# Optimization experiments

Measured on AMD Instinct MI355X. Metric: run time of the kernel, lower is better.

The kernel has to match this reference:

```python
import jax, jax.numpy as jnp
import numpy as np

N_HEAD = 16
SCALE = True


def setup_inputs() -> dict:
    key = jax.random.key(0)
    k1, k2, k3 = jax.random.split(key, 3)
    B, S, D = 4, 2048, 1024
    x = jax.random.normal(k1, (B, S, D), dtype=jnp.float32)
    w_attn = jax.random.normal(k2, (D, 3 * D), dtype=jnp.float32) * 0.02
    b_attn = jnp.zeros((3 * D,), dtype=jnp.float32)
    w_proj = jax.random.normal(k3, (D, D), dtype=jnp.float32) * 0.02
    b_proj = jnp.zeros((D,), dtype=jnp.float32)
    return {"x": x, "w_attn": w_attn, "b_attn": b_attn, "w_proj": w_proj, "b_proj": b_proj}


def reference(x, w_attn, b_attn, w_proj, b_proj):
    B, S, D = x.shape
    H = N_HEAD
    hd = D // H
    qkv = x @ w_attn + b_attn  # [B,S,3D] (Conv1D)
    q, k, v = jnp.split(qkv, 3, axis=-1)
    # split heads -> [B,H,S,hd]
    q = q.reshape(B, S, H, hd).transpose(0, 2, 1, 3)
    k = k.reshape(B, S, H, hd).transpose(0, 2, 1, 3)
    v = v.reshape(B, S, H, hd).transpose(0, 2, 1, 3)
    w = jnp.einsum('bhqd,bhkd->bhqk', q, k)  # [B,H,S,S]
    if SCALE:
        w = w / jnp.sqrt(jnp.asarray(hd, dtype=w.dtype))
    # causal mask exactly as in source: w*b + -10000*(1-b)
    bmask = jnp.tril(jnp.ones((S, S), dtype=w.dtype))[None, None]
    w = w * bmask + (-10000.0) * (1.0 - bmask)
    w = jax.nn.softmax(w, axis=-1)
    a = jnp.einsum('bhqk,bhkd->bhqd', w, v)  # [B,H,S,hd]
    a = a.transpose(0, 2, 1, 3).reshape(B, S, D)  # merge heads
    out = a @ w_proj + b_proj
    return out
```

## Files before the change

kernel.cpp:

```cpp
#include <hip/hip_runtime.h>

typedef __attribute__((ext_vector_type(8))) _Float16 f16x8;
typedef __attribute__((ext_vector_type(2))) __fp16 h16x2;
typedef __attribute__((ext_vector_type(4))) float f32x4;

#define S_LEN 2048
#define DMODEL 1024
#define NHEAD 16
#define HD 64
#define QKV_LD 3072
#define BTOT 4
#define LOG2E 1.4426950408889634f

#define GLL16(g, l)                                              \
  __builtin_amdgcn_global_load_lds(                              \
      (const __attribute__((address_space(1))) void*)(g),        \
      (__attribute__((address_space(3))) void*)(l), 16, 0, 0)

#define MFMA16(a, b, c) __builtin_amdgcn_mfma_f32_16x16x32_f16(a, b, c, 0, 0, 0)

__global__ __launch_bounds__(256) void cvt_f32_f16_k(const float* __restrict__ in,
                                                     _Float16* __restrict__ out, int n) {
  int i = (blockIdx.x * 256 + threadIdx.x) * 4;
  int stride = gridDim.x * 256 * 4;
  for (; i < n; i += stride) {
    float4 v = *(const float4*)(in + i);
    _Float16 h[4];
    h[0] = (_Float16)v.x; h[1] = (_Float16)v.y; h[2] = (_Float16)v.z; h[3] = (_Float16)v.w;
    *(uint2*)(out + i) = *(const uint2*)h;
  }
}

__global__ __launch_bounds__(256) void transpose_cvt_k(const float* __restrict__ W,
                                                       _Float16* __restrict__ Wt,
                                                       int K, int N) {
  __shared__ float t[32][33];
  int n0 = blockIdx.x * 32, k0 = blockIdx.y * 32;
  int tx = threadIdx.x, ty = threadIdx.y;
#pragma unroll
  for (int i = 0; i < 32; i += 8)
    t[ty + i][tx] = W[(size_t)(k0 + ty + i) * N + n0 + tx];
  __syncthreads();
#pragma unroll
  for (int i = 0; i < 32; i += 8)
    Wt[(size_t)(n0 + ty + i) * K + k0 + tx] = (_Float16)t[tx][ty + i];
}

template <int OUT_F32>
__global__ __launch_bounds__(256) void gemm_bt_k(const _Float16* __restrict__ A,
                                                 const _Float16* __restrict__ Bt,
                                                 const float* __restrict__ bias,
                                                 void* __restrict__ C,
                                                 int M, int N, int K) {
  __shared__ _Float16 As[128 * 64];
  __shared__ _Float16 Bs[128 * 64];
  const int tid = threadIdx.x;
  const int wid = tid >> 6, lane = tid & 63;
  const int quad = lane >> 4, l16 = lane & 15;
  const int wr = wid >> 1, wc = wid & 1;

  const int lin = blockIdx.y * gridDim.x + blockIdx.x;
  const int width = 8 * gridDim.x;
  const int group = lin / width;
  const int pm = group * 8 + (lin % width) % 8;
  const int pn = (lin % width) / 8;
  const int tm = pm * 128, tn = pn * 128;

  const int row0 = tid >> 3;
  const int xc = 8 * ((tid & 7) ^ (row0 & 7));
  const _Float16* Ag = A + (size_t)(tm + row0) * K + xc;
  const _Float16* Bg = Bt + (size_t)(tn + row0) * K + xc;
  _Float16* AsW = &As[wid * 512];
  _Float16* BsW = &Bs[wid * 512];

  f32x4 acc[4][4] = {};

  for (int k0 = 0; k0 < K; k0 += 64) {
    __syncthreads();
#pragma unroll
    for (int p = 0; p < 4; p++) {
      GLL16(Ag + k0 + (size_t)(32 * p) * K, AsW + 2048 * p);
      GLL16(Bg + k0 + (size_t)(32 * p) * K, BsW + 2048 * p);
    }
    __syncthreads();

#pragma unroll
    for (int ks = 0; ks < 2; ks++) {
      f16x8 af[4], bf[4];
#pragma unroll
      for (int mt = 0; mt < 4; mt++)
        af[mt] = *(const f16x8*)&As[(wr * 64 + mt * 16 + l16) * 64 +
                                    (((ks * 4 + quad) ^ (l16 & 7)) << 3)];
#pragma unroll
      for (int nt = 0; nt < 4; nt++)
        bf[nt] = *(const f16x8*)&Bs[(wc * 64 + nt * 16 + l16) * 64 +
                                    (((ks * 4 + quad) ^ (l16 & 7)) << 3)];
#pragma unroll
      for (int mt = 0; mt < 4; mt++)
#pragma unroll
        for (int nt = 0; nt < 4; nt++)
          acc[mt][nt] = MFMA16(af[mt], bf[nt], acc[mt][nt]);
    }
  }

#pragma unroll
  for (int nt = 0; nt < 4; nt++) {
    int col = tn + wc * 64 + nt * 16 + l16;
    float bv = bias[col];
#pragma unroll
    for (int mt = 0; mt < 4; mt++) {
      int row = tm + wr * 64 + mt * 16 + quad * 4;
#pragma unroll
      for (int r = 0; r < 4; r++) {
        float v = acc[mt][nt][r] + bv;
        if (OUT_F32)
          ((float*)C)[(size_t)(row + r) * N + col] = v;
        else
          ((_Float16*)C)[(size_t)(row + r) * N + col] = (_Float16)v;
      }
    }
  }
}

__global__ __launch_bounds__(512, 4) void attn_k(const _Float16* __restrict__ qkv,
                                                 _Float16* __restrict__ out) {
  __shared__ __align__(16) char pool[53760];
  _Float16* KsB = (_Float16*)pool;
  _Float16* VTsB = (_Float16*)(pool + 16384);

  const int tid = threadIdx.x, wid = tid >> 6, lane = tid & 63;
  const int quad = lane >> 4, l16 = lane & 15;
  const int qg = wid & 3, kg = wid >> 2;
  _Float16* PsW = (_Float16*)(pool + 32768) + wid * 1280;
  const int bh = blockIdx.x, b = bh >> 4, h = bh & 15;
  const int p = blockIdx.y;
  const _Float16* base = qkv + (size_t)b * S_LEN * QKV_LD + h * HD;

  const int krow = tid >> 3;
  const _Float16* Kg = base + DMODEL + (size_t)krow * QKV_LD +
                       8 * ((tid & 7) ^ (krow & 7));
  const bool vstager = (tid < 256);
  const int kp = tid & 31, dbase = ((tid >> 5) & 7) * 8;
  const _Float16* Vg = base + 2 * DMODEL + (size_t)(2 * kp) * QKV_LD + dbase;

  int voff[8];
#pragma unroll
  for (int i = 0; i < 8; i++) {
    int d = dbase + i;
    voff[i] = d * 32 + (((kp >> 2) ^ (d & 7)) << 2) + (kp & 3);
  }

  auto stage_V = [&](int bufi, uint4 v0, uint4 v1) {
    union { uint4 u; _Float16 h[8]; } a, c;
    a.u = v0; c.u = v1;
    uint* VT32 = (uint*)(VTsB + bufi * 4096);
#pragma unroll
    for (int i = 0; i < 8; i++) {
      union { _Float16 h[2]; uint u; } w;
      w.h[0] = a.h[i]; w.h[1] = c.h[i];
      VT32[voff[i]] = w.u;
    }
  };

  auto run_pass = [&](int qt) {
    f16x8 bq[2][2];
    {
      const _Float16 qs = (_Float16)(0.125f * LOG2E);
#pragma unroll
      for (int nt = 0; nt < 2; nt++)
#pragma unroll
        for (int ks = 0; ks < 2; ks++) {
          union { uint4 u; f16x8 h; } v;
          v.u = *(const uint4*)(base +
                                (size_t)(qt + qg * 32 + nt * 16 + l16) * QKV_LD +
                                ks * 32 + quad * 8);
          bq[nt][ks] = v.h * qs;
        }
    }

    float l_i[2] = {0.f, 0.f};
    f32x4 o[4][2] = {};

    const int qmin_w = qt + qg * 32;
    const int qmax_w = qmin_w + 31;
    const int nj = qt / 64 + 2;

    __syncthreads();
    GLL16(Kg, KsB + wid * 512);
    if (vstager) stage_V(0, *(const uint4*)(Vg), *(const uint4*)(Vg + QKV_LD));
    __syncthreads();

    for (int j = 0; j < nj; j++) {
      const int cur = j & 1, nxt = cur ^ 1;
      const int k0g = j * 64;
      const bool pf = (j + 1 < nj);
      uint4 pv0, pv1;
      if (pf) {
        const int kn = k0g + 64;
        GLL16(Kg + (size_t)kn * QKV_LD, KsB + nxt * 4096 + wid * 512);
        if (vstager) {
          pv0 = *(const uint4*)(Vg + (size_t)kn * QKV_LD);
          pv1 = *(const uint4*)(Vg + (size_t)(kn + 1) * QKV_LD);
        }
      }

      const int kgbase = k0g + kg * 32;
      if (kgbase <= qmax_w) {
        const _Float16* Kc = KsB + cur * 4096;
        f32x4 sc[2][2];
#pragma unroll
        for (int mt = 0; mt < 2; mt++)
#pragma unroll
          for (int nt = 0; nt < 2; nt++)
            sc[mt][nt] = f32x4{-4.f, -4.f, -4.f, -4.f};
#pragma unroll
        for (int ks = 0; ks < 2; ks++)
#pragma unroll
          for (int mt = 0; mt < 2; mt++) {
            f16x8 ak = *(const f16x8*)&Kc[(kg * 32 + mt * 16 + l16) * 64 +
                                          (((ks * 4 + quad) ^ (l16 & 7)) << 3)];
            sc[mt][0] = MFMA16(ak, bq[0][ks], sc[mt][0]);
            sc[mt][1] = MFMA16(ak, bq[1][ks], sc[mt][1]);
          }

        const bool need_mask = (kgbase + 31 > qmin_w);
#pragma unroll
        for (int nt = 0; nt < 2; nt++) {
          const int qgl = qmin_w + nt * 16 + l16;
          float pe[8];
#pragma unroll
          for (int mt = 0; mt < 2; mt++)
#pragma unroll
            for (int r = 0; r < 4; r++) {
              float v = sc[mt][nt][r];
              if (need_mask) {
                int kgi = kgbase + mt * 16 + quad * 4 + r;
                v = (kgi <= qgl) ? v : -3.0e38f;
              }
              pe[mt * 4 + r] = __builtin_amdgcn_exp2f(v);
            }
          l_i[nt] += ((pe[0] + pe[1]) + (pe[2] + pe[3])) +
                     ((pe[4] + pe[5]) + (pe[6] + pe[7]));
#pragma unroll
          for (int mt = 0; mt < 2; mt++) {
            union { h16x2 h[2]; uint2 u; } w;
            w.h[0] = __builtin_amdgcn_cvt_pkrtz(pe[mt * 4 + 0], pe[mt * 4 + 1]);
            w.h[1] = __builtin_amdgcn_cvt_pkrtz(pe[mt * 4 + 2], pe[mt * 4 + 3]);
            *(uint2*)&PsW[(nt * 16 + l16) * 40 + mt * 16 + quad * 4] = w.u;
          }
        }

        const _Float16* Vc = VTsB + cur * 4096;
        f16x8 bp0 = *(const f16x8*)&PsW[l16 * 40 + quad * 8];
        f16x8 bp1 = *(const f16x8*)&PsW[(16 + l16) * 40 + quad * 8];
#pragma unroll
        for (int md = 0; md < 4; md++) {
          f16x8 av = *(const f16x8*)&Vc[(md * 16 + l16) * 64 +
                                        (((kg * 4 + quad) ^ (l16 & 7)) << 3)];
          o[md][0] = MFMA16(av, bp0, o[md][0]);
          o[md][1] = MFMA16(av, bp1, o[md][1]);
        }
      }

      if (pf && vstager) stage_V(nxt, pv0, pv1);
      __syncthreads();
    }

#pragma unroll
    for (int nt = 0; nt < 2; nt++) {
      float r = l_i[nt];
      r += __shfl_xor(r, 16, 64);
      r += __shfl_xor(r, 32, 64);
      l_i[nt] = r;
    }
    float* X = (float*)pool;
    float* ML = (float*)(pool + 53248);
    if (kg == 1) {
#pragma unroll
      for (int md = 0; md < 4; md++)
#pragma unroll
        for (int nt = 0; nt < 2; nt++)
          *(f32x4*)&X[qg * 2048 + (md * 2 + nt) * 256 + lane * 4] = o[md][nt];
      if (quad == 0) {
#pragma unroll
        for (int nt = 0; nt < 2; nt++)
          ML[(qg * 2 + nt) * 16 + l16] = l_i[nt];
      }
    }
    __syncthreads();
    if (kg == 0) {
      _Float16* PsE = (_Float16*)(pool + 32768) + qg * 2304;
      float inv[2];
#pragma unroll
      for (int nt = 0; nt < 2; nt++)
        inv[nt] = 1.0f / (l_i[nt] + ML[(qg * 2 + nt) * 16 + l16]);
#pragma unroll
      for (int md = 0; md < 4; md++)
#pragma unroll
        for (int nt = 0; nt < 2; nt++) {
          f32x4 o1 = *(const f32x4*)&X[qg * 2048 + (md * 2 + nt) * 256 + lane * 4];
          f32x4 ot = o[md][nt] + o1;
          union { h16x2 h[2]; uint2 u; } w;
          w.h[0] = __builtin_amdgcn_cvt_pkrtz(ot[0] * inv[nt], ot[1] * inv[nt]);
          w.h[1] = __builtin_amdgcn_cvt_pkrtz(ot[2] * inv[nt], ot[3] * inv[nt]);
          *(uint2*)&PsE[(nt * 16 + l16) * 72 + md * 16 + quad * 4] = w.u;
        }
      {
        int r = lane >> 1, ch = (lane & 1) * 32;
        const int qgl = qt + qg * 32 + r;
        _Float16* orow = out + (size_t)(b * S_LEN + qgl) * DMODEL + h * HD + ch;
#pragma unroll
        for (int i = 0; i < 4; i++)
          *(uint4*)(orow + i * 8) = *(const uint4*)&PsE[r * 72 + ch + i * 8];
      }
    }
  };

  run_pass(p * 128);
  run_pass((15 - p) * 128);
}

extern "C" void kernel_launch(void* const* d_in, const int* in_sizes, int n_in,
                              void* d_out, int out_size, void* d_ws, size_t ws_size,
                              hipStream_t stream) {
  const float* x = (const float*)d_in[0];
  const float* w_attn = (const float*)d_in[1];
  const float* b_attn = (const float*)d_in[2];
  const float* w_proj = (const float*)d_in[3];
  const float* b_proj = (const float*)d_in[4];
  float* outp = (float*)d_out;

  char* ws = (char*)d_ws;
  _Float16* x16 = (_Float16*)ws;
  _Float16* wTa = (_Float16*)(ws + 16777216);
  _Float16* wTp = (_Float16*)(ws + 16777216 + 6291456);
  _Float16* qkv = (_Float16*)(ws + 25165824);
  _Float16* abuf = (_Float16*)(ws + 75497472);

  const int nx = BTOT * S_LEN * DMODEL;

  cvt_f32_f16_k<<<8192, 256, 0, stream>>>(x, x16, nx);
  transpose_cvt_k<<<dim3(QKV_LD / 32, DMODEL / 32), dim3(32, 8), 0, stream>>>(
      w_attn, wTa, DMODEL, QKV_LD);
  transpose_cvt_k<<<dim3(DMODEL / 32, DMODEL / 32), dim3(32, 8), 0, stream>>>(
      w_proj, wTp, DMODEL, DMODEL);

  gemm_bt_k<0><<<dim3(QKV_LD / 128, BTOT * S_LEN / 128), 256, 0, stream>>>(
      x16, wTa, b_attn, qkv, BTOT * S_LEN, QKV_LD, DMODEL);

  attn_k<<<dim3(BTOT * NHEAD, 8), 512, 0, stream>>>(qkv, abuf);

  gemm_bt_k<1><<<dim3(DMODEL / 128, BTOT * S_LEN / 128), 256, 0, stream>>>(
      abuf, wTp, b_proj, outp, BTOT * S_LEN, DMODEL, DMODEL);
}
```

Before: 255.2 us.

## Add 256x256-tile double-buffered GEMM kernel for QKV projection

Adds a new GEMM kernel with 256x256 output tiles over 8 waves, used for the QKV projection. It double-buffers LDS loads through global_load_lds with an XOR-swizzled layout, remaps block order into groups of 8 rows for L2 reuse, and raises wave priority around the MFMA bursts. Larger tiles raise arithmetic intensity per byte loaded. The cost is 128 KB of LDS per block, 128 accumulator registers per thread, and only 384 blocks in the grid, which limits occupancy and load balance.

```diff
diff --git a/kernel.cpp b/kernel.cpp
--- a/kernel.cpp
+++ b/kernel.cpp
@@ -118,6 +118,104 @@
         else
           ((_Float16*)C)[(size_t)(row + r) * N + col] = (_Float16)v;
       }
+    }
+  }
+}
+
+__global__ __launch_bounds__(512, 2) void gemm256_k(const _Float16* __restrict__ A,
+                                                    const _Float16* __restrict__ Bt,
+                                                    const float* __restrict__ bias,
+                                                    _Float16* __restrict__ C,
+                                                    int M, int N, int K) {
+  __shared__ __align__(16) _Float16 sb[2][2][16384];
+  const int tid = threadIdx.x;
+  const int wid = tid >> 6, lane = tid & 63;
+  const int quad = lane >> 4, l16 = lane & 15;
+  const int wm = wid >> 2, wn = wid & 3;
+
+  const int lin = blockIdx.y * gridDim.x + blockIdx.x;
+  const int width = 8 * gridDim.x;
+  const int group = lin / width;
+  const int pm = group * 8 + (lin % width) % 8;
+  const int pn = (lin % width) / 8;
+  const int tm = pm * 256, tn = pn * 256;
+
+  const int row0 = tid >> 3;
+  const int xc = 8 * ((tid & 7) ^ (row0 & 7));
+  const _Float16* Ag = A + (size_t)(tm + row0) * K + xc;
+  const _Float16* Bg = Bt + (size_t)(tn + row0) * K + xc;
+
+  f32x4 acc[8][4] = {};
+  const int ntk = K >> 6;
+
+  auto stage = [&](int t) {
+    const int d = t & 1;
+    const int k0 = t << 6;
+#pragma unroll
+    for (int r = 0; r < 4; r++) {
+      GLL16(Ag + k0 + (size_t)(64 * r) * K, &sb[d][0][r * 4096 + wid * 512]);
+      GLL16(Bg + k0 + (size_t)(64 * r) * K, &sb[d][1][r * 4096 + wid * 512]);
+    }
+  };
+
+  stage(0);
+  if (ntk > 1) stage(1);
+
+  for (int t = 0; t < ntk; t++) {
+    if (t + 1 < ntk)
+      asm volatile("s_waitcnt vmcnt(8)" ::: "memory");
+    else
+      asm volatile("s_waitcnt vmcnt(0)" ::: "memory");
+    __builtin_amdgcn_s_barrier();
+    asm volatile("" ::: "memory");
+    __builtin_amdgcn_sched_barrier(0);
+
+    const _Float16* As_ = sb[t & 1][0];
+    const _Float16* Bs_ = sb[t & 1][1];
+    f16x8 bf[4][2];
+#pragma unroll
+    for (int n = 0; n < 4; n++)
+#pragma unroll
+      for (int ks = 0; ks < 2; ks++)
+        bf[n][ks] = *(const f16x8*)&Bs_[(wn * 64 + n * 16 + l16) * 64 +
+                                        (((ks * 4 + quad) ^ (l16 & 7)) << 3)];
+#pragma unroll
+    for (int mh = 0; mh < 2; mh++) {
+      f16x8 af[4][2];
+#pragma unroll
+      for (int m = 0; m < 4; m++)
+#pragma unroll
+        for (int ks = 0; ks < 2; ks++)
+          af[m][ks] =
+              *(const f16x8*)&As_[(wm * 128 + mh * 64 + m * 16 + l16) * 64 +
+                                  (((ks * 4 + quad) ^ (l16 & 7)) << 3)];
+      __builtin_amdgcn_s_setprio(1);
+#pragma unroll
+      for (int ks = 0; ks < 2; ks++)
+#pragma unroll
+        for (int m = 0; m < 4; m++)
+#pragma unroll
+          for (int n = 0; n < 4; n++)
+            acc[mh * 4 + m][n] = MFMA16(af[m][ks], bf[n][ks], acc[mh * 4 + m][n]);
+      __builtin_amdgcn_s_setprio(0);
+    }
+
+    __builtin_amdgcn_s_barrier();
+    asm volatile("" ::: "memory");
+    __builtin_amdgcn_sched_barrier(0);
+    if (t + 2 < ntk) stage(t + 2);
+  }
+
+#pragma unroll
+  for (int n = 0; n < 4; n++) {
+    int col = tn + wn * 64 + n * 16 + l16;
+    float bv = bias[col];
+#pragma unroll
+    for (int m8 = 0; m8 < 8; m8++) {
+      int row = tm + wm * 128 + m8 * 16 + quad * 4;
+#pragma unroll
+      for (int r = 0; r < 4; r++)
+        C[(size_t)(row + r) * N + col] = (_Float16)(acc[m8][n][r] + bv);
     }
   }
 }
@@ -345,7 +443,7 @@
   transpose_cvt_k<<<dim3(DMODEL / 32, DMODEL / 32), dim3(32, 8), 0, stream>>>(
       w_proj, wTp, DMODEL, DMODEL);
 
-  gemm_bt_k<0><<<dim3(QKV_LD / 128, BTOT * S_LEN / 128), 256, 0, stream>>>(
+  gemm256_k<<<dim3(QKV_LD / 256, BTOT * S_LEN / 256), 512, 0, stream>>>(
       x16, wTa, b_attn, qkv, BTOT * S_LEN, QKV_LD, DMODEL);
 
   attn_k<<<dim3(BTOT * NHEAD, 8), 512, 0, stream>>>(qkv, abuf);
```

Result: no change. 257.5 us (+0.9%).

## Software-pipeline attention loop: overlap QK of next tile with softmax-PV of previous

Applied to the files above, without the earlier changes.

Restructures the causal attention inner loop into a two-stage software pipeline. The QK^T MFMAs for tile j now run in the same step as the softmax and PV MFMAs for tile j-1, with score accumulators alternating between two register sets. V gets a triple-buffered LDS staging area, which grows shared memory from about 53.8KB to about 62KB. The aim is to hide exp/softmax latency behind MFMA work, at the cost of more registers and LDS, which may reduce occupancy under the 512x4 launch bounds.

```diff
diff --git a/kernel.cpp b/kernel.cpp
--- a/kernel.cpp
+++ b/kernel.cpp
@@ -124,14 +124,14 @@
 
 __global__ __launch_bounds__(512, 4) void attn_k(const _Float16* __restrict__ qkv,
                                                  _Float16* __restrict__ out) {
-  __shared__ __align__(16) char pool[53760];
+  __shared__ __align__(16) char pool[61952];
   _Float16* KsB = (_Float16*)pool;
   _Float16* VTsB = (_Float16*)(pool + 16384);
 
   const int tid = threadIdx.x, wid = tid >> 6, lane = tid & 63;
   const int quad = lane >> 4, l16 = lane & 15;
   const int qg = wid & 3, kg = wid >> 2;
-  _Float16* PsW = (_Float16*)(pool + 32768) + wid * 1280;
+  _Float16* PsW = (_Float16*)(pool + 40960) + wid * 1280;
   const int bh = blockIdx.x, b = bh >> 4, h = bh & 15;
   const int p = blockIdx.y;
   const _Float16* base = qkv + (size_t)b * S_LEN * QKV_LD + h * HD;
@@ -161,6 +161,71 @@
       VT32[voff[i]] = w.u;
     }
   };
+
+#define QK_SEC(J, SCN)                                                        \
+  {                                                                           \
+    const int kgb_ = (J) * 64 + kg * 32;                                      \
+    if (kgb_ <= qmax_w) {                                                     \
+      const _Float16* Kc = KsB + ((J) & 1) * 4096;                            \
+      _Pragma("unroll")                                                       \
+      for (int mt = 0; mt < 2; mt++) {                                        \
+        SCN[mt][0] = f32x4{-4.f, -4.f, -4.f, -4.f};                           \
+        SCN[mt][1] = f32x4{-4.f, -4.f, -4.f, -4.f};                           \
+      }                                                                       \
+      _Pragma("unroll")                                                       \
+      for (int ks = 0; ks < 2; ks++)                                          \
+        _Pragma("unroll")                                                     \
+        for (int mt = 0; mt < 2; mt++) {                                      \
+          f16x8 ak = *(const f16x8*)&Kc[(kg * 32 + mt * 16 + l16) * 64 +      \
+                                        (((ks * 4 + quad) ^ (l16 & 7)) << 3)];\
+          SCN[mt][0] = MFMA16(ak, bq[0][ks], SCN[mt][0]);                     \
+          SCN[mt][1] = MFMA16(ak, bq[1][ks], SCN[mt][1]);                     \
+        }                                                                     \
+    }                                                                         \
+  }
+
+#define SM_PV(JP, SCO, VB)                                                    \
+  {                                                                           \
+    const int kgb_ = (JP) * 64 + kg * 32;                                     \
+    if (kgb_ <= qmax_w) {                                                     \
+      const bool need_mask = (kgb_ + 31 > qmin_w);                            \
+      _Pragma("unroll")                                                       \
+      for (int nt = 0; nt < 2; nt++) {                                        \
+        const int qgl = qmin_w + nt * 16 + l16;                               \
+        float pe[8];                                                          \
+        _Pragma("unroll")                                                     \
+        for (int mt = 0; mt < 2; mt++)                                        \
+          _Pragma("unroll")                                                   \
+          for (int r = 0; r < 4; r++) {                                       \
+            float v = SCO[mt][nt][r];                                         \
+            if (need_mask) {                                                  \
+              int kgi = kgb_ + mt * 16 + quad * 4 + r;                        \
+              v = (kgi <= qgl) ? v : -3.0e38f;                                \
+            }                                                                 \
+            pe[mt * 4 + r] = __builtin_amdgcn_exp2f(v);                       \
+          }                                                                   \
+        l_i[nt] += ((pe[0] + pe[1]) + (pe[2] + pe[3])) +                      \
+                   ((pe[4] + pe[5]) + (pe[6] + pe[7]));                       \
+        _Pragma("unroll")                                                     \
+        for (int mt = 0; mt < 2; mt++) {                                      \
+          union { h16x2 hh[2]; uint2 u; } w;                                  \
+          w.hh[0] = __builtin_amdgcn_cvt_pkrtz(pe[mt * 4 + 0], pe[mt * 4 + 1]);\
+          w.hh[1] = __builtin_amdgcn_cvt_pkrtz(pe[mt * 4 + 2], pe[mt * 4 + 3]);\
+          *(uint2*)&PsW[(nt * 16 + l16) * 40 + mt * 16 + quad * 4] = w.u;     \
+        }                                                                     \
+      }                                                                       \
+      const _Float16* Vc = VTsB + (VB) * 4096;                                \
+      f16x8 bp0 = *(const f16x8*)&PsW[l16 * 40 + quad * 8];                   \
+      f16x8 bp1 = *(const f16x8*)&PsW[(16 + l16) * 40 + quad * 8];            \
+      _Pragma("unroll")                                                       \
+      for (int md = 0; md < 4; md++) {                                        \
+        f16x8 av = *(const f16x8*)&Vc[(md * 16 + l16) * 64 +                  \
+                                      (((kg * 4 + quad) ^ (l16 & 7)) << 3)];  \
+        o[md][0] = MFMA16(av, bp0, o[md][0]);                                 \
+        o[md][1] = MFMA16(av, bp1, o[md][1]);                                 \
+      }                                                                       \
+    }                                                                         \
+  }
 
   auto run_pass = [&](int qt) {
     f16x8 bq[2][2];
@@ -180,6 +245,7 @@
 
     float l_i[2] = {0.f, 0.f};
     f32x4 o[4][2] = {};
+    f32x4 scA[2][2], scB[2][2];
 
     const int qmin_w = qt + qg * 32;
     const int qmax_w = qmin_w + 31;
@@ -190,81 +256,43 @@
     if (vstager) stage_V(0, *(const uint4*)(Vg), *(const uint4*)(Vg + QKV_LD));
     __syncthreads();
 
-    for (int j = 0; j < nj; j++) {
-      const int cur = j & 1, nxt = cur ^ 1;
-      const int k0g = j * 64;
-      const bool pf = (j + 1 < nj);
-      uint4 pv0, pv1;
-      if (pf) {
-        const int kn = k0g + 64;
-        GLL16(Kg + (size_t)kn * QKV_LD, KsB + nxt * 4096 + wid * 512);
+    int vm1 = 2, v0 = 0, vp1 = 1;
+
+    for (int j = 0; j < nj; j += 2) {
+      {
+        const int kn = j * 64 + 64;
+        uint4 pv0, pv1;
+        GLL16(Kg + (size_t)kn * QKV_LD, KsB + ((j + 1) & 1) * 4096 + wid * 512);
         if (vstager) {
           pv0 = *(const uint4*)(Vg + (size_t)kn * QKV_LD);
           pv1 = *(const uint4*)(Vg + (size_t)(kn + 1) * QKV_LD);
         }
-      }
-
-      const int kgbase = k0g + kg * 32;
-      if (kgbase <= qmax_w) {
-        const _Float16* Kc = KsB + cur * 4096;
-        f32x4 sc[2][2];
-#pragma unroll
-        for (int mt = 0; mt < 2; mt++)
-#pragma unroll
-          for (int nt = 0; nt < 2; nt++)
-            sc[mt][nt] = f32x4{-4.f, -4.f, -4.f, -4.f};
-#pragma unroll
-        for (int ks = 0; ks < 2; ks++)
-#pragma unroll
-          for (int mt = 0; mt < 2; mt++) {
-            f16x8 ak = *(const f16x8*)&Kc[(kg * 32 + mt * 16 + l16) * 64 +
-                                          (((ks * 4 + quad) ^ (l16 & 7)) << 3)];
-            sc[mt][0] = MFMA16(ak, bq[0][ks], sc[mt][0]);
-            sc[mt][1] = MFMA16(ak, bq[1][ks], sc[mt][1]);
-          }
-
-        const bool need_mask = (kgbase + 31 > qmin_w);
-#pragma unroll
-        for (int nt = 0; nt < 2; nt++) {
-          const int qgl = qmin_w + nt * 16 + l16;
-          float pe[8];
-#pragma unroll
-          for (int mt = 0; mt < 2; mt++)
-#pragma unroll
-            for (int r = 0; r < 4; r++) {
-              float v = sc[mt][nt][r];
-              if (need_mask) {
-                int kgi = kgbase + mt * 16 + quad * 4 + r;
-                v = (kgi <= qgl) ? v : -3.0e38f;
-              }
-              pe[mt * 4 + r] = __builtin_amdgcn_exp2f(v);
-            }
-          l_i[nt] += ((pe[0] + pe[1]) + (pe[2] + pe[3])) +
-                     ((pe[4] + pe[5]) + (pe[6] + pe[7]));
-#pragma unroll
-          for (int mt = 0; mt < 2; mt++) {
-            union { h16x2 h[2]; uint2 u; } w;
-            w.h[0] = __builtin_amdgcn_cvt_pkrtz(pe[mt * 4 + 0], pe[mt * 4 + 1]);
-            w.h[1] = __builtin_amdgcn_cvt_pkrtz(pe[mt * 4 + 2], pe[mt * 4 + 3]);
-            *(uint2*)&PsW[(nt * 16 + l16) * 40 + mt * 16 + quad * 4] = w.u;
+        QK_SEC(j, scA);
+        if (j > 0) SM_PV(j - 1, scB, vm1);
+        if (vstager) stage_V(vp1, pv0, pv1);
+        __syncthreads();
+        int t = vm1; vm1 = v0; v0 = vp1; vp1 = t;
+      }
+      {
+        const bool pf = (j + 2 < nj);
+        uint4 pv0, pv1;
+        if (pf) {
+          const int kn = (j + 1) * 64 + 64;
+          GLL16(Kg + (size_t)kn * QKV_LD, KsB + (j & 1) * 4096 + wid * 512);
+          if (vstager) {
+            pv0 = *(const uint4*)(Vg + (size_t)kn * QKV_LD);
+            pv1 = *(const uint4*)(Vg + (size_t)(kn + 1) * QKV_LD);
           }
         }
-
-        const _Float16* Vc = VTsB + cur * 4096;
-        f16x8 bp0 = *(const f16x8*)&PsW[l16 * 40 + quad * 8];
-        f16x8 bp1 = *(const f16x8*)&PsW[(16 + l16) * 40 + quad * 8];
-#pragma unroll
-        for (int md = 0; md < 4; md++) {
-          f16x8 av = *(const f16x8*)&Vc[(md * 16 + l16) * 64 +
-                                        (((kg * 4 + quad) ^ (l16 & 7)) << 3)];
-          o[md][0] = MFMA16(av, bp0, o[md][0]);
-          o[md][1] = MFMA16(av, bp1, o[md][1]);
-        }
-      }
-
-      if (pf && vstager) stage_V(nxt, pv0, pv1);
-      __syncthreads();
-    }
+        QK_SEC(j + 1, scB);
+        SM_PV(j, scA, vm1);
+        if (pf && vstager) stage_V(vp1, pv0, pv1);
+        __syncthreads();
+        int t = vm1; vm1 = v0; v0 = vp1; vp1 = t;
+      }
+    }
+    SM_PV(nj - 1, scB, vm1);
+    __syncthreads();
 
 #pragma unroll
     for (int nt = 0; nt < 2; nt++) {
@@ -274,7 +302,7 @@
       l_i[nt] = r;
     }
     float* X = (float*)pool;
-    float* ML = (float*)(pool + 53248);
+    float* ML = (float*)(pool + 61440);
     if (kg == 1) {
 #pragma unroll
       for (int md = 0; md < 4; md++)
@@ -289,7 +317,7 @@
     }
     __syncthreads();
     if (kg == 0) {
-      _Float16* PsE = (_Float16*)(pool + 32768) + qg * 2304;
+      _Float16* PsE = (_Float16*)(pool + 40960) + qg * 2304;
       float inv[2];
 #pragma unroll
       for (int nt = 0; nt < 2; nt++)
@@ -300,9 +328,9 @@
         for (int nt = 0; nt < 2; nt++) {
           f32x4 o1 = *(const f32x4*)&X[qg * 2048 + (md * 2 + nt) * 256 + lane * 4];
           f32x4 ot = o[md][nt] + o1;
-          union { h16x2 h[2]; uint2 u; } w;
-          w.h[0] = __builtin_amdgcn_cvt_pkrtz(ot[0] * inv[nt], ot[1] * inv[nt]);
-          w.h[1] = __builtin_amdgcn_cvt_pkrtz(ot[2] * inv[nt], ot[3] * inv[nt]);
+          union { h16x2 hh[2]; uint2 u; } w;
+          w.hh[0] = __builtin_amdgcn_cvt_pkrtz(ot[0] * inv[nt], ot[1] * inv[nt]);
+          w.hh[1] = __builtin_amdgcn_cvt_pkrtz(ot[2] * inv[nt], ot[3] * inv[nt]);
           *(uint2*)&PsE[(nt * 16 + l16) * 72 + md * 16 + quad * 4] = w.u;
         }
       {
```

New measurement: 444.0 us. 74.0% more time.
